# Performance work log

Measured on AMD Instinct MI355X. Metric: run time of the kernel, lower is better.

Reference implementation:

```python
import jax, jax.numpy as jnp
import numpy as np

N_HEADS = 8
EPS = 1e-6


def setup_inputs() -> dict:
    key = jax.random.key(0)
    ks = jax.random.split(key, 9)
    B, L, E = 4, 4096, 512
    s = 1.0 / np.sqrt(E)
    return {
        "x": jax.random.normal(ks[0], (B, L, E), jnp.float32),
        "Wq": jax.random.normal(ks[1], (E, E), jnp.float32) * s,
        "bq": jax.random.normal(ks[2], (E,), jnp.float32) * 0.01,
        "Wk": jax.random.normal(ks[3], (E, E), jnp.float32) * s,
        "bk": jax.random.normal(ks[4], (E,), jnp.float32) * 0.01,
        "Wv": jax.random.normal(ks[5], (E, E), jnp.float32) * s,
        "bv": jax.random.normal(ks[6], (E,), jnp.float32) * 0.01,
        "Wo": jax.random.normal(ks[7], (E, E), jnp.float32) * s,
        "bo": jax.random.normal(ks[8], (E,), jnp.float32) * 0.01,
    }


def reference(x, Wq, bq, Wk, bk, Wv, bv, Wo, bo):
    # x: (B, L, E); self-attention so query = key = value = x
    B, L, E = x.shape
    H = N_HEADS
    d = E // H
    m = jnp.float32(L)  # m = max(src_len, tgt_len)

    # projections (torch Linear: x @ W.T + b), then ReLU feature map
    q = jax.nn.relu(x @ Wq.T + bq).reshape(B, L, H, d)
    k = jax.nn.relu(x @ Wk.T + bk).reshape(B, L, H, d)
    v = (x @ Wv.T + bv).reshape(B, L, H, d)

    # cosFormer positional reweighting: (pi/2) * i / m for i = 1..L
    idx = (jnp.pi / 2.0) * jnp.arange(1, L + 1, dtype=jnp.float32) / m  # (L,)
    sin = jnp.sin(idx)[None, :, None, None]  # (1, L, 1, 1)
    cos = jnp.cos(idx)[None, :, None, None]

    q_sin, q_cos = q * sin, q * cos
    k_sin, k_cos = k * sin, k * cos

    # non-causal linear attention: per-head kv state, O(L * d^2)
    kv_cos = jnp.einsum("blhk,blhd->bhkd", k_cos, v)  # (B, H, d, d)
    kv_sin = jnp.einsum("blhk,blhd->bhkd", k_sin, v)

    k_cos_sum = k_cos.sum(axis=1)  # (B, H, d)
    k_sin_sum = k_sin.sum(axis=1)

    z = 1.0 / jnp.maximum(
        jnp.einsum("blhd,bhd->blh", q_cos, k_cos_sum)
        + jnp.einsum("blhd,bhd->blh", q_sin, k_sin_sum),
        EPS,
    )  # (B, L, H)

    attn = (
        jnp.einsum("blhk,bhkd->blhd", q_cos, kv_cos)
        + jnp.einsum("blhk,bhkd->blhd", q_sin, kv_sin)
    ) * z[..., None]

    out = attn.reshape(B, L, E) @ Wo.T + bo  # (B, L, E)
    return out
```

## Files before the change

kernel.cpp:

```cpp
#include <hip/hip_runtime.h>
#include <hip/hip_bf16.h>

#define L_SEQ 4096
#define E_DIM 512
#define NHEAD 8
#define DHEAD 64
#define NBATCH 4
#define NROWS (NBATCH * L_SEQ)

typedef short bf16x8 __attribute__((ext_vector_type(8)));
typedef float f32x4 __attribute__((ext_vector_type(4)));

__device__ __forceinline__ float bf2f(ushort u) {
    union { float f; unsigned int i; } x;
    x.i = ((unsigned int)u) << 16;
    return x.f;
}
__device__ __forceinline__ ushort f2bf(float f) {
    unsigned int u = __float_as_uint(f);
    unsigned int r = 0x7fffu + ((u >> 16) & 1u);
    u += r;
    return (ushort)(u >> 16);
}

#define GLD16(gptr, lptr) \
    __builtin_amdgcn_global_load_lds( \
        (const __attribute__((address_space(1))) void*)(gptr), \
        (__attribute__((address_space(3))) void*)(lptr), 16, 0, 0)

__global__ void convert_kernel(const float* __restrict__ in, ushort* __restrict__ out, int n4) {
    int stride = gridDim.x * blockDim.x;
    for (int i = blockIdx.x * blockDim.x + threadIdx.x; i < n4; i += stride) {
        float4 f = reinterpret_cast<const float4*>(in)[i];
        ushort4 o;
        o.x = f2bf(f.x); o.y = f2bf(f.y); o.z = f2bf(f.z); o.w = f2bf(f.w);
        reinterpret_cast<ushort4*>(out)[i] = o;
    }
}

__global__ __launch_bounds__(256) void convert_w_kernel(
    const float* __restrict__ w0, const float* __restrict__ w1,
    const float* __restrict__ w2, const float* __restrict__ w3,
    ushort* __restrict__ o0, ushort* __restrict__ o1,
    ushort* __restrict__ o2, ushort* __restrict__ o3,
    float* __restrict__ sintab, float* __restrict__ costab)
{
    const int tid = threadIdx.x;
    const int y = blockIdx.y;
    if (y == 4) {
        const int l = blockIdx.x * 256 + tid;
        if (blockIdx.x < 16) {
            const float ang = (float)(l + 1) * (1.5707963267948966f / (float)L_SEQ);
            sintab[l] = sinf(ang);
            costab[l] = cosf(ang);
        }
        return;
    }
    const float* in = (y == 0) ? w0 : (y == 1) ? w1 : (y == 2) ? w2 : w3;
    ushort* out = (y == 0) ? o0 : (y == 1) ? o1 : (y == 2) ? o2 : o3;
    const int i = blockIdx.x * 256 + tid;
    float4 f = reinterpret_cast<const float4*>(in)[i];
    ushort4 o;
    o.x = f2bf(f.x); o.y = f2bf(f.y); o.z = f2bf(f.z); o.w = f2bf(f.w);
    reinterpret_cast<ushort4*>(out)[i] = o;
}

__global__ __launch_bounds__(512) void gemm2_kernel(
    int modeBase,
    const ushort* __restrict__ xA, const ushort* __restrict__ oA,
    const ushort* __restrict__ wq, const ushort* __restrict__ wk,
    const ushort* __restrict__ wv, const ushort* __restrict__ wo,
    const float* __restrict__ bq, const float* __restrict__ bk,
    const float* __restrict__ bv, const float* __restrict__ bo,
    const float* __restrict__ sintab, const float* __restrict__ costab,
    ushort* __restrict__ qc, ushort* __restrict__ qs,
    ushort* __restrict__ kcT, ushort* __restrict__ ksT, ushort* __restrict__ vT,
    float* __restrict__ outF)
{
    __shared__ ushort SH[49152];

    const int tid = threadIdx.x;
    const int lane = tid & 63;
    const int wid = tid >> 6;
    const int wm = wid >> 2;
    const int wn = wid & 3;
    const int mode = modeBase + (blockIdx.y >> 1);
    const int colBase = (blockIdx.y & 1) * 256;
    const int rowBase = blockIdx.x * 128;

    const ushort* __restrict__ A = (mode == 3) ? oA : xA;
    const ushort* __restrict__ W = (mode == 0) ? wq : (mode == 1) ? wk : (mode == 2) ? wv : wo;
    const float* __restrict__ bias = (mode == 0) ? bq : (mode == 1) ? bk : (mode == 2) ? bv : bo;

    const int fr = lane & 15;
    const int g = lane >> 4;
    const int fr7 = fr & 7;

    const int sc_row = tid >> 3;
    const int sc_ch  = tid & 7;

    f32x4 acc[4][4];
#pragma unroll
    for (int m = 0; m < 4; ++m)
#pragma unroll
        for (int n = 0; n < 4; ++n)
            acc[m][n] = (f32x4){0.f, 0.f, 0.f, 0.f};

    auto STAGE = [&](int kt, int bufb) {
        const int k0 = kt * 64;
#pragma unroll
        for (int i = 0; i < 2; ++i) {
            const int row = i * 64 + sc_row;
            const int srcc = (sc_ch ^ (row & 7)) * 8;
            GLD16(&A[(size_t)(rowBase + row) * E_DIM + k0 + srcc],
                  &SH[bufb + (i * 512 + tid) * 8]);
        }
#pragma unroll
        for (int i = 0; i < 4; ++i) {
            const int row = i * 64 + sc_row;
            const int srcc = (sc_ch ^ (row & 7)) * 8;
            GLD16(&W[(size_t)(colBase + row) * E_DIM + k0 + srcc],
                  &SH[bufb + 8192 + (i * 512 + tid) * 8]);
        }
    };

    STAGE(0, 0);
    STAGE(1, 24576);
    asm volatile("s_waitcnt vmcnt(6)" ::: "memory");
    __builtin_amdgcn_sched_barrier(0);
    __builtin_amdgcn_s_barrier();
    __builtin_amdgcn_sched_barrier(0);

    const int kch0 = (g ^ fr7) * 8;
    const int kch1 = ((4 + g) ^ fr7) * 8;
    const int aroff = (wm * 64 + fr) * 64;
    const int broff = 8192 + (wn * 64 + fr) * 64;

    for (int t = 0; t < 8; ++t) {
        const int base = (t & 1) * 24576;
        bf16x8 af[2][4], bfv[2][4];
#pragma unroll
        for (int m = 0; m < 4; ++m) {
            af[0][m] = *reinterpret_cast<const bf16x8*>(&SH[base + aroff + m * 1024 + kch0]);
            af[1][m] = *reinterpret_cast<const bf16x8*>(&SH[base + aroff + m * 1024 + kch1]);
        }
#pragma unroll
        for (int n = 0; n < 4; ++n) {
            bfv[0][n] = *reinterpret_cast<const bf16x8*>(&SH[base + broff + n * 1024 + kch0]);
            bfv[1][n] = *reinterpret_cast<const bf16x8*>(&SH[base + broff + n * 1024 + kch1]);
        }
        asm volatile("s_waitcnt lgkmcnt(0)" ::: "memory");
        __builtin_amdgcn_sched_barrier(0);
        __builtin_amdgcn_s_barrier();
        __builtin_amdgcn_sched_barrier(0);

        if (t + 2 < 8) STAGE(t + 2, base);

        __builtin_amdgcn_s_setprio(1);
#pragma unroll
        for (int kk = 0; kk < 2; ++kk)
#pragma unroll
            for (int m = 0; m < 4; ++m)
#pragma unroll
                for (int n = 0; n < 4; ++n)
                    acc[m][n] = __builtin_amdgcn_mfma_f32_16x16x32_bf16(
                        af[kk][m], bfv[kk][n], acc[m][n], 0, 0, 0);
        __builtin_amdgcn_s_setprio(0);
        __builtin_amdgcn_sched_barrier(0);

        if (t < 7) {
            if (t < 6) asm volatile("s_waitcnt vmcnt(6)" ::: "memory");
            else       asm volatile("s_waitcnt vmcnt(0)" ::: "memory");
            __builtin_amdgcn_sched_barrier(0);
            __builtin_amdgcn_s_barrier();
            __builtin_amdgcn_sched_barrier(0);
        }
    }

    if (mode == 0) {
#pragma unroll
        for (int m = 0; m < 4; ++m) {
#pragma unroll
            for (int j = 0; j < 4; ++j) {
                const int grow = rowBase + wm * 64 + m * 16 + g * 4 + j;
                const int l = grow & (L_SEQ - 1);
                const float cv = costab[l], sv = sintab[l];
#pragma unroll
                for (int n = 0; n < 4; ++n) {
                    const int gcol = colBase + wn * 64 + n * 16 + fr;
                    float val = fmaxf(acc[m][n][j] + bias[gcol], 0.f);
                    const size_t oidx = (size_t)grow * E_DIM + gcol;
                    qc[oidx] = f2bf(val * cv);
                    qs[oidx] = f2bf(val * sv);
                }
            }
        }
    } else if (mode == 3) {
#pragma unroll
        for (int m = 0; m < 4; ++m) {
#pragma unroll
            for (int j = 0; j < 4; ++j) {
                const int grow = rowBase + wm * 64 + m * 16 + g * 4 + j;
#pragma unroll
                for (int n = 0; n < 4; ++n) {
                    const int gcol = colBase + wn * 64 + n * 16 + fr;
                    outF[(size_t)grow * E_DIM + gcol] = acc[m][n][j] + bias[gcol];
                }
            }
        }
    } else {
        ushort* TS = SH;
#pragma unroll
        for (int m = 0; m < 4; ++m) {
#pragma unroll
            for (int j = 0; j < 4; ++j) {
                const int lr_ = wm * 64 + m * 16 + g * 4 + j;
#pragma unroll
                for (int n = 0; n < 4; ++n) {
                    const int fc_ = wn * 64 + n * 16 + fr;
                    float val = acc[m][n][j] + bias[colBase + fc_];
                    if (mode == 1) val = fmaxf(val, 0.f);
                    TS[fc_ * 136 + lr_] = f2bf(val);
                }
            }
        }
        __syncthreads();
        const int b = rowBase >> 12;
        const int lloc = rowBase & (L_SEQ - 1);
#pragma unroll
        for (int i = 0; i < 8; ++i) {
            const int c = i * 512 + tid;
            const int r = c >> 4;
            const int cc = c & 15;
            const int gfeat = colBase + r;
            const size_t dst = ((size_t)(b * E_DIM + gfeat)) * L_SEQ + lloc + cc * 8;
            uint4 raw = *reinterpret_cast<const uint4*>(&TS[r * 136 + cc * 8]);
            if (mode == 2) {
                *reinterpret_cast<uint4*>(&vT[dst]) = raw;
            } else {
                ushort u[8] = {
                    (ushort)(raw.x & 0xffffu), (ushort)(raw.x >> 16),
                    (ushort)(raw.y & 0xffffu), (ushort)(raw.y >> 16),
                    (ushort)(raw.z & 0xffffu), (ushort)(raw.z >> 16),
                    (ushort)(raw.w & 0xffffu), (ushort)(raw.w >> 16)};
                const int lbase = lloc + cc * 8;
                float4 cv0 = *reinterpret_cast<const float4*>(&costab[lbase]);
                float4 cv1 = *reinterpret_cast<const float4*>(&costab[lbase + 4]);
                float4 sv0 = *reinterpret_cast<const float4*>(&sintab[lbase]);
                float4 sv1 = *reinterpret_cast<const float4*>(&sintab[lbase + 4]);
                const float cvv[8] = {cv0.x, cv0.y, cv0.z, cv0.w, cv1.x, cv1.y, cv1.z, cv1.w};
                const float svv[8] = {sv0.x, sv0.y, sv0.z, sv0.w, sv1.x, sv1.y, sv1.z, sv1.w};
                ushort uc[8], us[8];
#pragma unroll
                for (int e = 0; e < 8; ++e) {
                    const float v = bf2f(u[e]);
                    uc[e] = f2bf(v * cvv[e]);
                    us[e] = f2bf(v * svv[e]);
                }
                uint4 oc, os;
                oc.x = (uint)uc[0] | ((uint)uc[1] << 16); oc.y = (uint)uc[2] | ((uint)uc[3] << 16);
                oc.z = (uint)uc[4] | ((uint)uc[5] << 16); oc.w = (uint)uc[6] | ((uint)uc[7] << 16);
                os.x = (uint)us[0] | ((uint)us[1] << 16); os.y = (uint)us[2] | ((uint)us[3] << 16);
                os.z = (uint)us[4] | ((uint)us[5] << 16); os.w = (uint)us[6] | ((uint)us[7] << 16);
                *reinterpret_cast<uint4*>(&kcT[dst]) = oc;
                *reinterpret_cast<uint4*>(&ksT[dst]) = os;
            }
        }
    }
}

__global__ __launch_bounds__(256) void kv_kernel(
    const ushort* __restrict__ kcT, const ushort* __restrict__ ksT, const ushort* __restrict__ vT,
    float* __restrict__ kv_part, float* __restrict__ sum_part)
{
    const int chunk = blockIdx.x;
    const int bh = blockIdx.y;
    const int tid = threadIdx.x;
    const int lane = tid & 63;
    const int w = tid >> 6;
    const int fr = lane & 15;
    const int g = lane >> 4;

    const size_t tbase = (size_t)bh * 64 * L_SEQ;

    f32x4 acc[8], accS[8];
#pragma unroll
    for (int n = 0; n < 8; ++n) {
        acc[n] = (f32x4){0.f, 0.f, 0.f, 0.f};
        accS[n] = (f32x4){0.f, 0.f, 0.f, 0.f};
    }
    bf16x8 ones;
#pragma unroll
    for (int j = 0; j < 8; ++j) ones[j] = (short)0x3F80;

    const int lchunk = chunk * (L_SEQ / 8);
    for (int l0 = lchunk; l0 < lchunk + (L_SEQ / 8); l0 += 32) {
        const int col = l0 + g * 8;
        bf16x8 af = *reinterpret_cast<const bf16x8*>(&vT[tbase + (size_t)(w * 16 + fr) * L_SEQ + col]);
        bf16x8 bc[4], bs[4];
#pragma unroll
        for (int n = 0; n < 4; ++n) {
            bc[n] = *reinterpret_cast<const bf16x8*>(&kcT[tbase + (size_t)(n * 16 + fr) * L_SEQ + col]);
            bs[n] = *reinterpret_cast<const bf16x8*>(&ksT[tbase + (size_t)(n * 16 + fr) * L_SEQ + col]);
        }
#pragma unroll
        for (int n = 0; n < 4; ++n) {
            acc[n]      = __builtin_amdgcn_mfma_f32_16x16x32_bf16(af, bc[n], acc[n], 0, 0, 0);
            acc[n + 4]  = __builtin_amdgcn_mfma_f32_16x16x32_bf16(af, bs[n], acc[n + 4], 0, 0, 0);
            accS[n]     = __builtin_amdgcn_mfma_f32_16x16x32_bf16(ones, bc[n], accS[n], 0, 0, 0);
            accS[n + 4] = __builtin_amdgcn_mfma_f32_16x16x32_bf16(ones, bs[n], accS[n + 4], 0, 0, 0);
        }
    }

    const size_t pbase = ((size_t)(chunk * 32 + bh)) * 8192;
#pragma unroll
    for (int n = 0; n < 8; ++n)
#pragma unroll
        for (int j = 0; j < 4; ++j)
            kv_part[pbase + (size_t)(w * 16 + g * 4 + j) * 128 + n * 16 + fr] = acc[n][j];
    if (w == 0 && g == 0) {
        const size_t sbase = (size_t)(chunk * 32 + bh) * 128;
#pragma unroll
        for (int n = 0; n < 8; ++n)
            sum_part[sbase + n * 16 + fr] = accS[n][0];
    }
}

#define KVT_ROWS 80
#define KVT_STRIDE (KVT_ROWS * 128)
__global__ __launch_bounds__(256) void kv_reduce_kernel(
    const float* __restrict__ kv_part, const float* __restrict__ sum_part,
    ushort* __restrict__ kvT)
{
    const int bh = blockIdx.x;
    const int tid = threadIdx.x;
    ushort* kvb = kvT + (size_t)bh * KVT_STRIDE;
    for (int idx = tid; idx < 8192; idx += 256) {
        float s = 0.f;
#pragma unroll
        for (int c = 0; c < 8; ++c)
            s += kv_part[((size_t)(c * 32 + bh)) * 8192 + idx];
        kvb[idx] = f2bf(s);
    }
    if (tid < 128) {
        float s = 0.f;
#pragma unroll
        for (int c = 0; c < 8; ++c)
            s += sum_part[(size_t)(c * 32 + bh) * 128 + tid];
        const ushort hi = f2bf(s);
        const float lo = s - bf2f(hi);
        kvb[64 * 128 + tid] = hi;
        kvb[65 * 128 + tid] = f2bf(lo);
    }
    for (int idx = tid; idx < 14 * 128; idx += 256)
        kvb[66 * 128 + idx] = 0;
}

__global__ __launch_bounds__(256) void attn_kernel(
    const ushort* __restrict__ Qc, const ushort* __restrict__ Qs,
    const ushort* __restrict__ kvT,
    ushort* __restrict__ attn_out)
{
    const int bh = blockIdx.y;
    const int b = bh >> 3, h = bh & 7;
    const int tid = threadIdx.x;
    const int lane = tid & 63;
    const int w = tid >> 6;

    __shared__ ushort Bs[KVT_ROWS][136];

#pragma unroll
    for (int i = 0; i < 5; ++i) {
        const int c = i * 256 + tid;
        const int d = c >> 4, cc = c & 15;
        *reinterpret_cast<uint4*>(&Bs[d][cc * 8]) =
            *reinterpret_cast<const uint4*>(&kvT[(size_t)bh * KVT_STRIDE + (size_t)c * 8]);
    }
    __syncthreads();

    const int rowBase = blockIdx.x * 256 + w * 64;
    const int fr = lane & 15;
    const int g = lane >> 4;

    f32x4 acc[4][5];
#pragma unroll
    for (int m = 0; m < 4; ++m)
#pragma unroll
        for (int n = 0; n < 5; ++n)
            acc[m][n] = (f32x4){0.f, 0.f, 0.f, 0.f};

#pragma unroll
    for (int ks = 0; ks < 4; ++ks) {
        const ushort* __restrict__ src = (ks < 2) ? Qc : Qs;
        const int kk = (ks & 1) * 32 + g * 8;
        const int kcomb = ks * 32 + g * 8;

        bf16x8 af[4];
#pragma unroll
        for (int m = 0; m < 4; ++m) {
            const int r = rowBase + m * 16 + fr;
            af[m] = *reinterpret_cast<const bf16x8*>(
                &src[((size_t)(b * L_SEQ) + r) * E_DIM + h * DHEAD + kk]);
        }

        bf16x8 bfr[5];
#pragma unroll
        for (int n = 0; n < 5; ++n)
            bfr[n] = *reinterpret_cast<const bf16x8*>(&Bs[n * 16 + fr][kcomb]);
#pragma unroll
        for (int m = 0; m < 4; ++m)
#pragma unroll
            for (int n = 0; n < 5; ++n)
                acc[m][n] = __builtin_amdgcn_mfma_f32_16x16x32_bf16(af[m], bfr[n], acc[m][n], 0, 0, 0);
    }

#pragma unroll
    for (int m = 0; m < 4; ++m) {
#pragma unroll
        for (int j = 0; j < 4; ++j) {
            const float den = __shfl(acc[m][4][j], g * 16 + 0) + __shfl(acc[m][4][j], g * 16 + 1);
            const float z = 1.f / fmaxf(den, 1e-6f);
            const int grow = rowBase + m * 16 + g * 4 + j;
            const size_t obase = ((size_t)(b * L_SEQ) + grow) * E_DIM + h * DHEAD;
#pragma unroll
            for (int n = 0; n < 4; ++n)
                attn_out[obase + n * 16 + fr] = f2bf(acc[m][n][j] * z);
        }
    }
}

extern "C" void kernel_launch(void* const* d_in, const int* in_sizes, int n_in,
                              void* d_out, int out_size, void* d_ws, size_t ws_size,
                              hipStream_t stream) {
    const float* x  = (const float*)d_in[0];
    const float* Wq = (const float*)d_in[1];
    const float* bq = (const float*)d_in[2];
    const float* Wk = (const float*)d_in[3];
    const float* bk = (const float*)d_in[4];
    const float* Wv = (const float*)d_in[5];
    const float* bv = (const float*)d_in[6];
    const float* Wo = (const float*)d_in[7];
    const float* bo = (const float*)d_in[8];
    float* out = (float*)d_out;

    char* ws = (char*)d_ws;
    size_t off = 0;
    auto alloc = [&](size_t bytes) -> char* {
        char* p = ws + off;
        off += (bytes + 255) & ~(size_t)255;
        return p;
    };

    const size_t big = (size_t)NROWS * E_DIM * sizeof(ushort);
    ushort* xb  = (ushort*)alloc(big);
    ushort* wqb = (ushort*)alloc(512 * 512 * sizeof(ushort));
    ushort* wkb = (ushort*)alloc(512 * 512 * sizeof(ushort));
    ushort* wvb = (ushort*)alloc(512 * 512 * sizeof(ushort));
    ushort* wob = (ushort*)alloc(512 * 512 * sizeof(ushort));
    ushort* qc  = (ushort*)alloc(big);
    ushort* qs  = (ushort*)alloc(big);
    ushort* kcT = (ushort*)alloc(big);
    ushort* ksT = (ushort*)alloc(big);
    ushort* vT  = (ushort*)alloc(big);
    float* kv_part  = (float*)alloc((size_t)8 * 32 * 8192 * sizeof(float));
    float* sum_part = (float*)alloc((size_t)8 * 32 * 128 * sizeof(float));
    ushort* kvT     = (ushort*)alloc((size_t)32 * KVT_STRIDE * sizeof(ushort));
    float* sintab   = (float*)alloc(L_SEQ * sizeof(float));
    float* costab   = (float*)alloc(L_SEQ * sizeof(float));
    ushort* attnb = kcT;

    convert_kernel<<<2048, 256, 0, stream>>>(x, xb, NROWS * E_DIM / 4);
    convert_w_kernel<<<dim3(256, 5), 256, 0, stream>>>(
        Wq, Wk, Wv, Wo, wqb, wkb, wvb, wob, sintab, costab);

    gemm2_kernel<<<dim3(128, 6), 512, 0, stream>>>(
        0, xb, nullptr, wqb, wkb, wvb, wob, bq, bk, bv, bo,
        sintab, costab, qc, qs, kcT, ksT, vT, nullptr);

    kv_kernel<<<dim3(8, 32), 256, 0, stream>>>(kcT, ksT, vT, kv_part, sum_part);
    kv_reduce_kernel<<<32, 256, 0, stream>>>(kv_part, sum_part, kvT);

    attn_kernel<<<dim3(16, 32), 256, 0, stream>>>(qc, qs, kvT, attnb);

    gemm2_kernel<<<dim3(128, 2), 512, 0, stream>>>(
        3, xb, attnb, wqb, wkb, wvb, wob, bq, bk, bv, bo,
        sintab, costab, nullptr, nullptr, nullptr, nullptr, nullptr, out);
}
```

Before: 111.9 us.

## Defer sin/cos reweighting to consumers and fuse QKV projections per block

The QKV projection no longer writes separate cos- and sin-weighted copies of q and k. It writes a single q and a single transposed k, and the kv and attention kernels apply the positional weights on the fly from the tables. The projection kernel is also restructured so each block loops over all three weight matrices for one row tile. The A tile is reloaded per mode, and the grid drops from 768 to 256 blocks, each running a longer pipelined K loop with per-mode epilogues. This removes two full-size bf16 intermediate writes and reads. In exchange it adds extra conversion ALU work in the consumers, reduces parallelism in the projection, and requires more LDS per block.

```diff
diff --git a/kernel.cpp b/kernel.cpp
--- a/kernel.cpp
+++ b/kernel.cpp
@@ -27,6 +27,12 @@
     __builtin_amdgcn_global_load_lds( \
         (const __attribute__((address_space(1))) void*)(gptr), \
         (__attribute__((address_space(3))) void*)(lptr), 16, 0, 0)
+
+#define BAR_LGKM() do { \
+    asm volatile("s_waitcnt lgkmcnt(0)" ::: "memory"); \
+    __builtin_amdgcn_sched_barrier(0); \
+    __builtin_amdgcn_s_barrier(); \
+    __builtin_amdgcn_sched_barrier(0); } while (0)
 
 __global__ void convert_kernel(const float* __restrict__ in, ushort* __restrict__ out, int n4) {
     int stride = gridDim.x * blockDim.x;
@@ -65,39 +71,36 @@
     reinterpret_cast<ushort4*>(out)[i] = o;
 }
 
-__global__ __launch_bounds__(512) void gemm2_kernel(
-    int modeBase,
+__global__ __launch_bounds__(512) void gemm3_kernel(
+    int modeBase, int nt,
     const ushort* __restrict__ xA, const ushort* __restrict__ oA,
     const ushort* __restrict__ wq, const ushort* __restrict__ wk,
     const ushort* __restrict__ wv, const ushort* __restrict__ wo,
     const float* __restrict__ bq, const float* __restrict__ bk,
     const float* __restrict__ bv, const float* __restrict__ bo,
-    const float* __restrict__ sintab, const float* __restrict__ costab,
-    ushort* __restrict__ qc, ushort* __restrict__ qs,
-    ushort* __restrict__ kcT, ushort* __restrict__ ksT, ushort* __restrict__ vT,
+    ushort* __restrict__ qb, ushort* __restrict__ kT, ushort* __restrict__ vT,
     float* __restrict__ outF)
 {
-    __shared__ ushort SH[49152];
+    __shared__ ushort SH[66048];
+    ushort* TS = SH + 49152;
 
     const int tid = threadIdx.x;
     const int lane = tid & 63;
     const int wid = tid >> 6;
     const int wm = wid >> 2;
     const int wn = wid & 3;
-    const int mode = modeBase + (blockIdx.y >> 1);
-    const int colBase = (blockIdx.y & 1) * 256;
-    const int rowBase = blockIdx.x * 128;
-
-    const ushort* __restrict__ A = (mode == 3) ? oA : xA;
-    const ushort* __restrict__ W = (mode == 0) ? wq : (mode == 1) ? wk : (mode == 2) ? wv : wo;
-    const float* __restrict__ bias = (mode == 0) ? bq : (mode == 1) ? bk : (mode == 2) ? bv : bo;
+    const int p = blockIdx.x;
+    const int rowBase = (p >> 1) * 128;
+    const int colBase = (p & 1) * 256;
+
+    const ushort* __restrict__ Ap = (modeBase == 3) ? oA : xA;
 
     const int fr = lane & 15;
     const int g = lane >> 4;
     const int fr7 = fr & 7;
-
     const int sc_row = tid >> 3;
     const int sc_ch  = tid & 7;
+    const int totKt = nt * 8;
 
     f32x4 acc[4][4];
 #pragma unroll
@@ -106,13 +109,17 @@
         for (int n = 0; n < 4; ++n)
             acc[m][n] = (f32x4){0.f, 0.f, 0.f, 0.f};
 
-    auto STAGE = [&](int kt, int bufb) {
-        const int k0 = kt * 64;
+    auto STAGE = [&](int gt2) {
+        const int mode = modeBase + (gt2 >> 3);
+        const ushort* __restrict__ W =
+            (mode == 0) ? wq : (mode == 1) ? wk : (mode == 2) ? wv : wo;
+        const int k0 = (gt2 & 7) * 64;
+        const int bufb = (gt2 & 1) * 24576;
 #pragma unroll
         for (int i = 0; i < 2; ++i) {
             const int row = i * 64 + sc_row;
             const int srcc = (sc_ch ^ (row & 7)) * 8;
-            GLD16(&A[(size_t)(rowBase + row) * E_DIM + k0 + srcc],
+            GLD16(&Ap[(size_t)(rowBase + row) * E_DIM + k0 + srcc],
                   &SH[bufb + (i * 512 + tid) * 8]);
         }
 #pragma unroll
@@ -124,8 +131,8 @@
         }
     };
 
-    STAGE(0, 0);
-    STAGE(1, 24576);
+    STAGE(0);
+    STAGE(1);
     asm volatile("s_waitcnt vmcnt(6)" ::: "memory");
     __builtin_amdgcn_sched_barrier(0);
     __builtin_amdgcn_s_barrier();
@@ -135,9 +142,11 @@
     const int kch1 = ((4 + g) ^ fr7) * 8;
     const int aroff = (wm * 64 + fr) * 64;
     const int broff = 8192 + (wn * 64 + fr) * 64;
-
-    for (int t = 0; t < 8; ++t) {
-        const int base = (t & 1) * 24576;
+    const int b = rowBase >> 12;
+    const int lloc = rowBase & (L_SEQ - 1);
+
+    for (int gt = 0; gt < totKt; ++gt) {
+        const int base = (gt & 1) * 24576;
         bf16x8 af[2][4], bfv[2][4];
 #pragma unroll
         for (int m = 0; m < 4; ++m) {
@@ -149,12 +158,9 @@
             bfv[0][n] = *reinterpret_cast<const bf16x8*>(&SH[base + broff + n * 1024 + kch0]);
             bfv[1][n] = *reinterpret_cast<const bf16x8*>(&SH[base + broff + n * 1024 + kch1]);
         }
-        asm volatile("s_waitcnt lgkmcnt(0)" ::: "memory");
-        __builtin_amdgcn_sched_barrier(0);
-        __builtin_amdgcn_s_barrier();
-        __builtin_amdgcn_sched_barrier(0);
-
-        if (t + 2 < 8) STAGE(t + 2, base);
+        BAR_LGKM();
+
+        if (gt + 2 < totKt) STAGE(gt + 2);
 
         __builtin_amdgcn_s_setprio(1);
 #pragma unroll
@@ -168,109 +174,88 @@
         __builtin_amdgcn_s_setprio(0);
         __builtin_amdgcn_sched_barrier(0);
 
-        if (t < 7) {
-            if (t < 6) asm volatile("s_waitcnt vmcnt(6)" ::: "memory");
-            else       asm volatile("s_waitcnt vmcnt(0)" ::: "memory");
+        if ((gt & 7) == 7) {
+            const int mode = modeBase + (gt >> 3);
+            const float* __restrict__ bias =
+                (mode == 0) ? bq : (mode == 1) ? bk : (mode == 2) ? bv : bo;
+            if (mode == 0) {
+#pragma unroll
+                for (int m = 0; m < 4; ++m)
+#pragma unroll
+                    for (int j = 0; j < 4; ++j) {
+                        const int grow = rowBase + wm * 64 + m * 16 + g * 4 + j;
+#pragma unroll
+                        for (int n = 0; n < 4; ++n) {
+                            const int gcol = colBase + wn * 64 + n * 16 + fr;
+                            const float val = fmaxf(acc[m][n][j] + bias[gcol], 0.f);
+                            qb[(size_t)grow * E_DIM + gcol] = f2bf(val);
+                        }
+                    }
+            } else if (mode == 3) {
+#pragma unroll
+                for (int m = 0; m < 4; ++m)
+#pragma unroll
+                    for (int j = 0; j < 4; ++j) {
+                        const int grow = rowBase + wm * 64 + m * 16 + g * 4 + j;
+#pragma unroll
+                        for (int n = 0; n < 4; ++n) {
+                            const int gcol = colBase + wn * 64 + n * 16 + fr;
+                            outF[(size_t)grow * E_DIM + gcol] = acc[m][n][j] + bias[gcol];
+                        }
+                    }
+            } else {
+                ushort* __restrict__ dstbuf = (mode == 1) ? kT : vT;
+#pragma unroll
+                for (int ph = 0; ph < 2; ++ph) {
+                    BAR_LGKM();
+                    if ((wn >> 1) == ph) {
+#pragma unroll
+                        for (int m = 0; m < 4; ++m)
+#pragma unroll
+                            for (int j = 0; j < 4; ++j) {
+                                const int lr_ = wm * 64 + m * 16 + g * 4 + j;
+#pragma unroll
+                                for (int n = 0; n < 4; ++n) {
+                                    const int fcl = (wn & 1) * 64 + n * 16 + fr;
+                                    float val = acc[m][n][j] + bias[colBase + ph * 128 + fcl];
+                                    if (mode == 1) val = fmaxf(val, 0.f);
+                                    TS[fcl * 132 + lr_] = f2bf(val);
+                                }
+                            }
+                    }
+                    BAR_LGKM();
+#pragma unroll
+                    for (int i = 0; i < 4; ++i) {
+                        const int c = i * 512 + tid;
+                        const int r = c >> 4;
+                        const int cc = c & 15;
+                        const int gfeat = colBase + ph * 128 + r;
+                        const size_t dst = ((size_t)(b * E_DIM + gfeat)) * L_SEQ + lloc + cc * 8;
+                        *reinterpret_cast<uint4*>(&dstbuf[dst]) =
+                            *reinterpret_cast<const uint4*>(&TS[r * 132 + cc * 8]);
+                    }
+                }
+            }
+#pragma unroll
+            for (int m = 0; m < 4; ++m)
+#pragma unroll
+                for (int n = 0; n < 4; ++n)
+                    acc[m][n] = (f32x4){0.f, 0.f, 0.f, 0.f};
+        }
+
+        if (gt < totKt - 1) {
+            if (gt + 2 < totKt) asm volatile("s_waitcnt vmcnt(6)" ::: "memory");
+            else                asm volatile("s_waitcnt vmcnt(0)" ::: "memory");
             __builtin_amdgcn_sched_barrier(0);
             __builtin_amdgcn_s_barrier();
             __builtin_amdgcn_sched_barrier(0);
         }
     }
-
-    if (mode == 0) {
-#pragma unroll
-        for (int m = 0; m < 4; ++m) {
-#pragma unroll
-            for (int j = 0; j < 4; ++j) {
-                const int grow = rowBase + wm * 64 + m * 16 + g * 4 + j;
-                const int l = grow & (L_SEQ - 1);
-                const float cv = costab[l], sv = sintab[l];
-#pragma unroll
-                for (int n = 0; n < 4; ++n) {
-                    const int gcol = colBase + wn * 64 + n * 16 + fr;
-                    float val = fmaxf(acc[m][n][j] + bias[gcol], 0.f);
-                    const size_t oidx = (size_t)grow * E_DIM + gcol;
-                    qc[oidx] = f2bf(val * cv);
-                    qs[oidx] = f2bf(val * sv);
-                }
-            }
-        }
-    } else if (mode == 3) {
-#pragma unroll
-        for (int m = 0; m < 4; ++m) {
-#pragma unroll
-            for (int j = 0; j < 4; ++j) {
-                const int grow = rowBase + wm * 64 + m * 16 + g * 4 + j;
-#pragma unroll
-                for (int n = 0; n < 4; ++n) {
-                    const int gcol = colBase + wn * 64 + n * 16 + fr;
-                    outF[(size_t)grow * E_DIM + gcol] = acc[m][n][j] + bias[gcol];
-                }
-            }
-        }
-    } else {
-        ushort* TS = SH;
-#pragma unroll
-        for (int m = 0; m < 4; ++m) {
-#pragma unroll
-            for (int j = 0; j < 4; ++j) {
-                const int lr_ = wm * 64 + m * 16 + g * 4 + j;
-#pragma unroll
-                for (int n = 0; n < 4; ++n) {
-                    const int fc_ = wn * 64 + n * 16 + fr;
-                    float val = acc[m][n][j] + bias[colBase + fc_];
-                    if (mode == 1) val = fmaxf(val, 0.f);
-                    TS[fc_ * 136 + lr_] = f2bf(val);
-                }
-            }
-        }
-        __syncthreads();
-        const int b = rowBase >> 12;
-        const int lloc = rowBase & (L_SEQ - 1);
-#pragma unroll
-        for (int i = 0; i < 8; ++i) {
-            const int c = i * 512 + tid;
-            const int r = c >> 4;
-            const int cc = c & 15;
-            const int gfeat = colBase + r;
-            const size_t dst = ((size_t)(b * E_DIM + gfeat)) * L_SEQ + lloc + cc * 8;
-            uint4 raw = *reinterpret_cast<const uint4*>(&TS[r * 136 + cc * 8]);
-            if (mode == 2) {
-                *reinterpret_cast<uint4*>(&vT[dst]) = raw;
-            } else {
-                ushort u[8] = {
-                    (ushort)(raw.x & 0xffffu), (ushort)(raw.x >> 16),
-                    (ushort)(raw.y & 0xffffu), (ushort)(raw.y >> 16),
-                    (ushort)(raw.z & 0xffffu), (ushort)(raw.z >> 16),
-                    (ushort)(raw.w & 0xffffu), (ushort)(raw.w >> 16)};
-                const int lbase = lloc + cc * 8;
-                float4 cv0 = *reinterpret_cast<const float4*>(&costab[lbase]);
-                float4 cv1 = *reinterpret_cast<const float4*>(&costab[lbase + 4]);
-                float4 sv0 = *reinterpret_cast<const float4*>(&sintab[lbase]);
-                float4 sv1 = *reinterpret_cast<const float4*>(&sintab[lbase + 4]);
-                const float cvv[8] = {cv0.x, cv0.y, cv0.z, cv0.w, cv1.x, cv1.y, cv1.z, cv1.w};
-                const float svv[8] = {sv0.x, sv0.y, sv0.z, sv0.w, sv1.x, sv1.y, sv1.z, sv1.w};
-                ushort uc[8], us[8];
-#pragma unroll
-                for (int e = 0; e < 8; ++e) {
-                    const float v = bf2f(u[e]);
-                    uc[e] = f2bf(v * cvv[e]);
-                    us[e] = f2bf(v * svv[e]);
-                }
-                uint4 oc, os;
-                oc.x = (uint)uc[0] | ((uint)uc[1] << 16); oc.y = (uint)uc[2] | ((uint)uc[3] << 16);
-                oc.z = (uint)uc[4] | ((uint)uc[5] << 16); oc.w = (uint)uc[6] | ((uint)uc[7] << 16);
-                os.x = (uint)us[0] | ((uint)us[1] << 16); os.y = (uint)us[2] | ((uint)us[3] << 16);
-                os.z = (uint)us[4] | ((uint)us[5] << 16); os.w = (uint)us[6] | ((uint)us[7] << 16);
-                *reinterpret_cast<uint4*>(&kcT[dst]) = oc;
-                *reinterpret_cast<uint4*>(&ksT[dst]) = os;
-            }
-        }
-    }
 }
 
 __global__ __launch_bounds__(256) void kv_kernel(
-    const ushort* __restrict__ kcT, const ushort* __restrict__ ksT, const ushort* __restrict__ vT,
+    const ushort* __restrict__ kT, const ushort* __restrict__ vT,
+    const float* __restrict__ sintab, const float* __restrict__ costab,
     float* __restrict__ kv_part, float* __restrict__ sum_part)
 {
     const int chunk = blockIdx.x;
@@ -289,26 +274,36 @@
         acc[n] = (f32x4){0.f, 0.f, 0.f, 0.f};
         accS[n] = (f32x4){0.f, 0.f, 0.f, 0.f};
     }
-    bf16x8 ones;
-#pragma unroll
-    for (int j = 0; j < 8; ++j) ones[j] = (short)0x3F80;
 
     const int lchunk = chunk * (L_SEQ / 8);
     for (int l0 = lchunk; l0 < lchunk + (L_SEQ / 8); l0 += 32) {
         const int col = l0 + g * 8;
-        bf16x8 af = *reinterpret_cast<const bf16x8*>(&vT[tbase + (size_t)(w * 16 + fr) * L_SEQ + col]);
-        bf16x8 bc[4], bs[4];
+        bf16x8 vf = *reinterpret_cast<const bf16x8*>(&vT[tbase + (size_t)(w * 16 + fr) * L_SEQ + col]);
+        bf16x8 kf[4];
+#pragma unroll
+        for (int n = 0; n < 4; ++n)
+            kf[n] = *reinterpret_cast<const bf16x8*>(&kT[tbase + (size_t)(n * 16 + fr) * L_SEQ + col]);
+        float4 c0 = *reinterpret_cast<const float4*>(&costab[col]);
+        float4 c1 = *reinterpret_cast<const float4*>(&costab[col + 4]);
+        float4 s0 = *reinterpret_cast<const float4*>(&sintab[col]);
+        float4 s1 = *reinterpret_cast<const float4*>(&sintab[col + 4]);
+        const float c8[8] = {c0.x, c0.y, c0.z, c0.w, c1.x, c1.y, c1.z, c1.w};
+        const float s8[8] = {s0.x, s0.y, s0.z, s0.w, s1.x, s1.y, s1.z, s1.w};
+        bf16x8 afc, afs, cw, sw;
+#pragma unroll
+        for (int e = 0; e < 8; ++e) {
+            const float v = bf2f((ushort)vf[e]);
+            afc[e] = (short)f2bf(v * c8[e]);
+            afs[e] = (short)f2bf(v * s8[e]);
+            cw[e]  = (short)f2bf(c8[e]);
+            sw[e]  = (short)f2bf(s8[e]);
+        }
 #pragma unroll
         for (int n = 0; n < 4; ++n) {
-            bc[n] = *reinterpret_cast<const bf16x8*>(&kcT[tbase + (size_t)(n * 16 + fr) * L_SEQ + col]);
-            bs[n] = *reinterpret_cast<const bf16x8*>(&ksT[tbase + (size_t)(n * 16 + fr) * L_SEQ + col]);
-        }
-#pragma unroll
-        for (int n = 0; n < 4; ++n) {
-            acc[n]      = __builtin_amdgcn_mfma_f32_16x16x32_bf16(af, bc[n], acc[n], 0, 0, 0);
-            acc[n + 4]  = __builtin_amdgcn_mfma_f32_16x16x32_bf16(af, bs[n], acc[n + 4], 0, 0, 0);
-            accS[n]     = __builtin_amdgcn_mfma_f32_16x16x32_bf16(ones, bc[n], accS[n], 0, 0, 0);
-            accS[n + 4] = __builtin_amdgcn_mfma_f32_16x16x32_bf16(ones, bs[n], accS[n + 4], 0, 0, 0);
+            acc[n]      = __builtin_amdgcn_mfma_f32_16x16x32_bf16(afc, kf[n], acc[n], 0, 0, 0);
+            acc[n + 4]  = __builtin_amdgcn_mfma_f32_16x16x32_bf16(afs, kf[n], acc[n + 4], 0, 0, 0);
+            accS[n]     = __builtin_amdgcn_mfma_f32_16x16x32_bf16(cw,  kf[n], accS[n], 0, 0, 0);
+            accS[n + 4] = __builtin_amdgcn_mfma_f32_16x16x32_bf16(sw,  kf[n], accS[n + 4], 0, 0, 0);
         }
     }
 
@@ -357,8 +352,8 @@
 }
 
 __global__ __launch_bounds__(256) void attn_kernel(
-    const ushort* __restrict__ Qc, const ushort* __restrict__ Qs,
-    const ushort* __restrict__ kvT,
+    const ushort* __restrict__ Qb, const ushort* __restrict__ kvT,
+    const float* __restrict__ sintab, const float* __restrict__ costab,
     ushort* __restrict__ attn_out)
 {
     const int bh = blockIdx.y;
@@ -382,6 +377,14 @@
     const int fr = lane & 15;
     const int g = lane >> 4;
 
+    float cvm[4], svm[4];
+#pragma unroll
+    for (int m = 0; m < 4; ++m) {
+        const int l = (rowBase + m * 16 + fr) & (L_SEQ - 1);
+        cvm[m] = costab[l];
+        svm[m] = sintab[l];
+    }
+
     f32x4 acc[4][5];
 #pragma unroll
     for (int m = 0; m < 4; ++m)
@@ -391,7 +394,6 @@
 
 #pragma unroll
     for (int ks = 0; ks < 4; ++ks) {
-        const ushort* __restrict__ src = (ks < 2) ? Qc : Qs;
         const int kk = (ks & 1) * 32 + g * 8;
         const int kcomb = ks * 32 + g * 8;
 
@@ -399,8 +401,12 @@
 #pragma unroll
         for (int m = 0; m < 4; ++m) {
             const int r = rowBase + m * 16 + fr;
-            af[m] = *reinterpret_cast<const bf16x8*>(
-                &src[((size_t)(b * L_SEQ) + r) * E_DIM + h * DHEAD + kk]);
+            bf16x8 qf = *reinterpret_cast<const bf16x8*>(
+                &Qb[((size_t)(b * L_SEQ) + r) * E_DIM + h * DHEAD + kk]);
+            const float sc = (ks < 2) ? cvm[m] : svm[m];
+#pragma unroll
+            for (int e = 0; e < 8; ++e)
+                af[m][e] = (short)f2bf(bf2f((ushort)qf[e]) * sc);
         }
 
         bf16x8 bfr[5];
@@ -457,32 +463,30 @@
     ushort* wkb = (ushort*)alloc(512 * 512 * sizeof(ushort));
     ushort* wvb = (ushort*)alloc(512 * 512 * sizeof(ushort));
     ushort* wob = (ushort*)alloc(512 * 512 * sizeof(ushort));
-    ushort* qc  = (ushort*)alloc(big);
-    ushort* qs  = (ushort*)alloc(big);
-    ushort* kcT = (ushort*)alloc(big);
-    ushort* ksT = (ushort*)alloc(big);
+    ushort* qb  = (ushort*)alloc(big);
+    ushort* kT  = (ushort*)alloc(big);
     ushort* vT  = (ushort*)alloc(big);
     float* kv_part  = (float*)alloc((size_t)8 * 32 * 8192 * sizeof(float));
     float* sum_part = (float*)alloc((size_t)8 * 32 * 128 * sizeof(float));
     ushort* kvT     = (ushort*)alloc((size_t)32 * KVT_STRIDE * sizeof(ushort));
     float* sintab   = (float*)alloc(L_SEQ * sizeof(float));
     float* costab   = (float*)alloc(L_SEQ * sizeof(float));
-    ushort* attnb = kcT;
+    ushort* attnb = kT;
 
     convert_kernel<<<2048, 256, 0, stream>>>(x, xb, NROWS * E_DIM / 4);
     convert_w_kernel<<<dim3(256, 5), 256, 0, stream>>>(
         Wq, Wk, Wv, Wo, wqb, wkb, wvb, wob, sintab, costab);
 
-    gemm2_kernel<<<dim3(128, 6), 512, 0, stream>>>(
-        0, xb, nullptr, wqb, wkb, wvb, wob, bq, bk, bv, bo,
-        sintab, costab, qc, qs, kcT, ksT, vT, nullptr);
-
-    kv_kernel<<<dim3(8, 32), 256, 0, stream>>>(kcT, ksT, vT, kv_part, sum_part);
+    gemm3_kernel<<<256, 512, 0, stream>>>(
+        0, 3, xb, nullptr, wqb, wkb, wvb, wob, bq, bk, bv, bo,
+        qb, kT, vT, nullptr);
+
+    kv_kernel<<<dim3(8, 32), 256, 0, stream>>>(kT, vT, sintab, costab, kv_part, sum_part);
     kv_reduce_kernel<<<32, 256, 0, stream>>>(kv_part, sum_part, kvT);
 
-    attn_kernel<<<dim3(16, 32), 256, 0, stream>>>(qc, qs, kvT, attnb);
-
-    gemm2_kernel<<<dim3(128, 2), 512, 0, stream>>>(
-        3, xb, attnb, wqb, wkb, wvb, wob, bq, bk, bv, bo,
-        sintab, costab, nullptr, nullptr, nullptr, nullptr, nullptr, out);
-}
+    attn_kernel<<<dim3(16, 32), 256, 0, stream>>>(qb, kvT, sintab, costab, attnb);
+
+    gemm3_kernel<<<256, 512, 0, stream>>>(
+        3, 1, xb, attnb, wqb, wkb, wvb, wob, bq, bk, bv, bo,
+        nullptr, nullptr, nullptr, out);
+}
```

Measured after the change: 111.0 us. Within noise of the previous version (-0.8%).
